# Kernel optimization log

Measured on AMD Instinct MI355X. Metric: run time of the kernel, lower is better.

The kernel has to match this reference:

```python
import jax, jax.numpy as jnp
import numpy as np

N = 32          # agents_num
IN_DIM = 16     # node feature dim (excluding 2 pos cols)
HID = 128
HEADS = 4
OUT = 5
DUEL_H = 256
RADIUS = 0.3
LATENT = HID + HID * HEADS * 2  # 1152
BS = 128


def _lin(k, i, o):
    s = 1.0 / np.sqrt(i)
    return jax.random.uniform(k, (i, o), minval=-s, maxval=s, dtype=jnp.float32)


def setup_inputs() -> dict:
    key = jax.random.key(0)
    ks = jax.random.split(key, 16)
    pos = jax.random.uniform(ks[0], (BS, N, 2))
    feats = jax.random.normal(ks[1], (BS, N, IN_DIM))
    aidx = jax.random.randint(ks[2], (BS,), 0, N).astype(jnp.float32)
    node = jnp.concatenate([pos, feats], axis=-1).reshape(BS, N * (2 + IN_DIM))
    obs = jnp.concatenate([node, aidx[:, None]], axis=1)  # (BS, N*(2+IN_DIM)+1)
    return {
        "obs": obs,
        "enc_w1": _lin(ks[3], IN_DIM, HID), "enc_b1": jnp.zeros((HID,)),
        "enc_w2": _lin(ks[4], HID, HID), "enc_b2": jnp.zeros((HID,)),
        "wl1": _lin(ks[5], HID, HEADS * HID), "wr1": _lin(ks[6], HID, HEADS * HID),
        "att1": jax.random.normal(ks[7], (HEADS, HID)) * 0.1, "bias1": jnp.zeros((HEADS * HID,)),
        "wl2": _lin(ks[8], HID * HEADS, HEADS * HID), "wr2": _lin(ks[9], HID * HEADS, HEADS * HID),
        "att2": jax.random.normal(ks[10], (HEADS, HID)) * 0.1, "bias2": jnp.zeros((HEADS * HID,)),
        "q_w1": _lin(ks[11], LATENT, DUEL_H), "q_b1": jnp.zeros((DUEL_H,)),
        "q_w2": _lin(ks[12], DUEL_H, OUT), "q_b2": jnp.zeros((OUT,)),
        "v_w1": _lin(ks[13], LATENT, DUEL_H), "v_b1": jnp.zeros((DUEL_H,)),
        "v_w2": _lin(ks[14], DUEL_H, 1), "v_b2": jnp.zeros((1,)),
    }


def _gatv2(x, adj, wl, wr, att, bias):
    # Dense-masked GATv2 (PyG semantics: lin_l on source j, lin_r on target i,
    # leaky_relu(x_i + x_j) . att, softmax over neighbors j, aggregate lin_l(x_j)).
    bs, n, _ = x.shape
    gl = (x @ wl).reshape(bs, n, HEADS, HID)  # source transform
    gr = (x @ wr).reshape(bs, n, HEADS, HID)  # target transform
    e = jax.nn.leaky_relu(gr[:, :, None] + gl[:, None, :], 0.2)  # [b, i, j, h, c]
    logits = jnp.einsum('bijhc,hc->bijh', e, att)
    logits = jnp.where(adj[..., None], logits, -jnp.inf)  # diag always True (self loops)
    alpha = jax.nn.softmax(logits, axis=2)
    out = jnp.einsum('bijh,bjhc->bihc', alpha, gl).reshape(bs, n, HEADS * HID)
    return out + bias


def reference(obs, enc_w1, enc_b1, enc_w2, enc_b2,
              wl1, wr1, att1, bias1, wl2, wr2, att2, bias2,
              q_w1, q_b1, q_w2, q_b2, v_w1, v_b1, v_w2, v_b2):
    bs = obs.shape[0]
    node = obs[:, :-1].reshape(bs, N, 2 + IN_DIM)
    pos, feats = node[..., :2], node[..., 2:]
    aidx = jnp.clip(obs[:, -1], 0, N - 1).astype(jnp.int32)

    # radius_graph (per-graph, loop=False) + GATv2 add_self_loops => diag True
    d2 = jnp.sum((pos[:, :, None] - pos[:, None, :]) ** 2, axis=-1)  # [bs, N, N]
    adj = (d2 < RADIUS ** 2) | jnp.eye(N, dtype=bool)

    # encoder MLP then ReLU (as in forward)
    h = jax.nn.relu(feats @ enc_w1 + enc_b1)
    x = jax.nn.relu(h @ enc_w2 + enc_b2)  # [bs, N, HID]

    b = jnp.arange(bs)
    x1 = x[b, aidx]  # [bs, HID]

    x = jax.nn.relu(_gatv2(x, adj, wl1, wr1, att1, bias1))  # [bs, N, HID*HEADS]
    x2 = x[b, aidx]

    x = jax.nn.relu(_gatv2(x, adj, wl2, wr2, att2, bias2))
    x3 = x[b, aidx]

    x_cat = jnp.concatenate([x1, x2, x3], axis=1)  # [bs, LATENT]

    q = jax.nn.relu(x_cat @ q_w1 + q_b1) @ q_w2 + q_b2  # [bs, OUT]
    v = jax.nn.relu(x_cat @ v_w1 + v_b1) @ v_w2 + v_b2  # [bs, 1]
    return q - q.mean(axis=1, keepdims=True) + v
```

## Files before the change

### kernel.cpp

```cpp
#include <hip/hip_runtime.h>
#include <hip/hip_bf16.h>

typedef unsigned int uint_t;
typedef unsigned short ushort_t;
typedef __attribute__((ext_vector_type(8))) short short8;
typedef __attribute__((ext_vector_type(4))) float floatx4;

__device__ __forceinline__ float4 fma4(float4 a, float s, float4 w){
  a.x += s*w.x; a.y += s*w.y; a.z += s*w.z; a.w += s*w.w; return a;
}
__device__ __forceinline__ float4 relu4(float4 a){
  return make_float4(fmaxf(a.x,0.f),fmaxf(a.y,0.f),fmaxf(a.z,0.f),fmaxf(a.w,0.f));
}
__device__ __forceinline__ unsigned bf16rne(float f){
  unsigned u = __float_as_uint(f);
  return (u + 0x7fffu + ((u>>16)&1u)) >> 16;
}
__device__ __forceinline__ uint_t packbf(float f){
  unsigned hb = bf16rne(f);
  float hf = __uint_as_float(hb<<16);
  unsigned lb = bf16rne(f - hf);
  return (hb<<16) | lb;
}
__device__ __forceinline__ uint4 pack4(float4 v){
  uint4 u; u.x=packbf(v.x); u.y=packbf(v.y); u.z=packbf(v.z); u.w=packbf(v.w); return u;
}
__device__ __forceinline__ float unpk(uint_t u){
  return __uint_as_float(u & 0xffff0000u) + __uint_as_float(u<<16);
}
#define UNPACK8(u0,u1,hi,lo) \
  hi[0]=(short)(u0.x>>16); lo[0]=(short)u0.x; \
  hi[1]=(short)(u0.y>>16); lo[1]=(short)u0.y; \
  hi[2]=(short)(u0.z>>16); lo[2]=(short)u0.z; \
  hi[3]=(short)(u0.w>>16); lo[3]=(short)u0.w; \
  hi[4]=(short)(u1.x>>16); lo[4]=(short)u1.x; \
  hi[5]=(short)(u1.y>>16); lo[5]=(short)u1.y; \
  hi[6]=(short)(u1.z>>16); lo[6]=(short)u1.z; \
  hi[7]=(short)(u1.w>>16); lo[7]=(short)u1.w;


template<int NKC>
__device__ __forceinline__ void hgemm_body(
    const uint_t* __restrict__ xcatpk,
    const ushort_t* __restrict__ qw1Thi, const ushort_t* __restrict__ qw1Tlo,
    const ushort_t* __restrict__ vw1Thi, const ushort_t* __restrict__ vw1Tlo,
    float* __restrict__ part, int ks, int ct, int t, int k0c, int slot0)
{
  const int w = t>>6, lane = t&63, m = lane&15, quad = lane>>4;
  const ushort_t* Bhi = (ct<4) ? qw1Thi : vw1Thi;
  const int cbl = (ct<4) ? ct*64 : (ct-4)*64;
  const int cbg = (ct<4) ? ct*64 : 256 + (ct-4)*64;
  const int kb = k0c + ks*NKC;
  const uint_t* ap = xcatpk + (size_t)w*18432 + m*32 + quad*8 + (size_t)kb*512;
  const ushort_t* bp0 = Bhi + (size_t)((cbl>>4)+0)*18432 + m*32 + quad*8 + (size_t)kb*512;
  const ushort_t* bp1 = Bhi + (size_t)((cbl>>4)+1)*18432 + m*32 + quad*8 + (size_t)kb*512;
  const ushort_t* bp2 = Bhi + (size_t)((cbl>>4)+2)*18432 + m*32 + quad*8 + (size_t)kb*512;
  const ushort_t* bp3 = Bhi + (size_t)((cbl>>4)+3)*18432 + m*32 + quad*8 + (size_t)kb*512;
  const size_t lod = (size_t)(qw1Tlo - qw1Thi);
  floatx4 acc[4];
  #pragma unroll
  for (int i=0;i<4;i++) acc[i] = (floatx4){0.f,0.f,0.f,0.f};
  #pragma unroll
  for (int kc=0; kc<NKC; kc++){
    const uint4 ua0 = *(const uint4*)(ap);
    const uint4 ua1 = *(const uint4*)(ap+4);
    ap += 512;
    short8 ahi, alo;
    UNPACK8(ua0,ua1,ahi,alo)
    const ushort_t* bps[4] = {bp0, bp1, bp2, bp3};
    #pragma unroll
    for (int nt=0; nt<4; nt++){
      const short8 bh = *(const short8*)(bps[nt] + kc*512);
      const short8 bl = *(const short8*)(bps[nt] + kc*512 + lod);
      acc[nt] = __builtin_amdgcn_mfma_f32_16x16x32_bf16(ahi, bh, acc[nt], 0,0,0);
      acc[nt] = __builtin_amdgcn_mfma_f32_16x16x32_bf16(ahi, bl, acc[nt], 0,0,0);
      acc[nt] = __builtin_amdgcn_mfma_f32_16x16x32_bf16(alo, bh, acc[nt], 0,0,0);
    }
  }
  float* pdst = part + (size_t)(slot0+ks)*65536;
  const int crow0 = w*16 + quad*4;
  #pragma unroll
  for (int nt=0; nt<4; nt++){
    const int col = cbg + nt*16 + m;
    #pragma unroll
    for (int r=0;r<4;r++)
      pdst[(size_t)(crow0 + r)*512 + col] = acc[nt][r];
  }
}

__global__ __launch_bounds__(256) void prep_kernel(
    const float* __restrict__ obs,
    const float* __restrict__ enc_w1, const float* __restrict__ enc_b1,
    const float* __restrict__ enc_w2, const float* __restrict__ enc_b2,
    const float* __restrict__ wl1, const float* __restrict__ wr1,
    const float* __restrict__ wl2, const float* __restrict__ wr2,
    const float* __restrict__ q_w1, const float* __restrict__ v_w1,
    ushort_t* __restrict__ wl1Thi, ushort_t* __restrict__ wl1Tlo,
    ushort_t* __restrict__ wr1Thi, ushort_t* __restrict__ wr1Tlo,
    ushort_t* __restrict__ wl2Thi, ushort_t* __restrict__ wl2Tlo,
    ushort_t* __restrict__ wr2Thi, ushort_t* __restrict__ wr2Tlo,
    ushort_t* __restrict__ qw1Thi, ushort_t* __restrict__ qw1Tlo,
    ushort_t* __restrict__ vw1Thi, ushort_t* __restrict__ vw1Tlo,
    uint_t* __restrict__ xpk, uint_t* __restrict__ xcatpk,
    unsigned* __restrict__ adjw, int* __restrict__ aiw)
{
  const int t = threadIdx.x, bid = blockIdx.x;
  if (bid >= 512){
    __shared__ float sm[32][33];
    const int cw = bid - 512;
    const float* in; ushort_t* ohi; ushort_t* olo; int K, N, tt, ktiles;
    if (cw < 64)       { in=wl1;  ohi=wl1Thi; olo=wl1Tlo; K=128;  N=512; tt=cw;     ktiles=4;  }
    else if (cw < 128) { in=wr1;  ohi=wr1Thi; olo=wr1Tlo; K=128;  N=512; tt=cw-64;  ktiles=4;  }
    else if (cw < 384) { in=wl2;  ohi=wl2Thi; olo=wl2Tlo; K=512;  N=512; tt=cw-128; ktiles=16; }
    else if (cw < 640) { in=wr2;  ohi=wr2Thi; olo=wr2Tlo; K=512;  N=512; tt=cw-384; ktiles=16; }
    else if (cw < 800) { in=q_w1; ohi=qw1Thi; olo=qw1Tlo; K=1152; N=256; tt=cw-640; ktiles=20; }
    else               { in=v_w1; ohi=vw1Thi; olo=vw1Tlo; K=1152; N=256; tt=cw-800; ktiles=20; }
    const int kt = tt % ktiles, nt = tt / ktiles;
    const int r = t>>5, c = t&31;
    #pragma unroll
    for (int i=0;i<4;i++)
      sm[r+i*8][c] = in[(size_t)(kt*32 + r + i*8)*N + nt*32 + c];
    __syncthreads();
    #pragma unroll
    for (int i=0;i<4;i++){
      const int nl = r + i*8;
      const int n  = nt*32 + nl;
      const float f = sm[c][nl];
      const unsigned hb = bf16rne(f);
      const float hf = __uint_as_float(hb<<16);
      const unsigned lb = bf16rne(f - hf);
      const size_t off = (size_t)(n>>4)*(size_t)(16*K) + (size_t)kt*512 + (size_t)(n&15)*32 + c;
      ohi[off] = (ushort_t)hb;
      olo[off] = (ushort_t)lb;
    }
    return;
  }
  __shared__ float s_pos[64];
  __shared__ float s_feats[128];
  __shared__ __align__(16) float s_h[8*132];
  __shared__ int s_ai;
  const int s = bid & 127, g = bid >> 7;
  const float* ob = obs + s*577;

  if (t==0){
    float a = ob[576];
    a = fminf(fmaxf(a, 0.f), 31.f);
    s_ai = (int)a;
    if (g==0) aiw[s] = (int)a;
  }
  if (t < 128){ const int n=t>>4, f=t&15; s_feats[t] = ob[(g*8+n)*18+2+f]; }
  if (g==0 && t>=128 && t<192){ const int u=t-128; s_pos[u] = ob[(u>>1)*18 + (u&1)]; }
  __syncthreads();

  if (g==0 && t < 32){
    const float px = s_pos[2*t], py = s_pos[2*t+1];
    const float R2 = 0.09f;
    unsigned mm = 0u;
    for (int j=0;j<32;j++){
      const float dx = __fsub_rn(px, s_pos[2*j]), dy = __fsub_rn(py, s_pos[2*j+1]);
      const float d2 = __fadd_rn(__fmul_rn(dx,dx), __fmul_rn(dy,dy));
      if (d2 <= R2 || j==t) mm |= (1u<<j);
    }
    adjw[s*32+t] = mm;
  }

  const int n = t>>5, c0 = (t&31)*4;
  {
    float4 a = *(const float4*)(enc_b1+c0);
    #pragma unroll
    for (int f=0; f<16; f++)
      a = fma4(a, s_feats[n*16+f], *(const float4*)(enc_w1 + f*128 + c0));
    *(float4*)&s_h[n*132+c0] = relu4(a);
  }
  __syncthreads();
  {
    float4 a = *(const float4*)(enc_b2+c0);
    #pragma unroll 4
    for (int k=0;k<128;k+=4){
      const float4 hv = *(const float4*)&s_h[n*132+k];
      a = fma4(a, hv.x, *(const float4*)(enc_w2 + (k+0)*128 + c0));
      a = fma4(a, hv.y, *(const float4*)(enc_w2 + (k+1)*128 + c0));
      a = fma4(a, hv.z, *(const float4*)(enc_w2 + (k+2)*128 + c0));
      a = fma4(a, hv.w, *(const float4*)(enc_w2 + (k+3)*128 + c0));
    }
    a = relu4(a);
    const uint4 p = pack4(a);
    const int i = g*8 + n;
    uint_t* xp = xpk + (size_t)(s*2 + (i>>4))*2048 + (c0>>5)*512 + (i&15)*32 + (c0&31);
    *(uint4*)xp = p;
    if (i == s_ai){
      uint_t* xc = xcatpk + (size_t)(s>>4)*18432 + (c0>>5)*512 + (s&15)*32 + (c0&31);
      *(uint4*)xc = p;
    }
  }
}

__global__ __launch_bounds__(512) void pa1_kernel(
    const uint_t* __restrict__ xpk,
    const ushort_t* __restrict__ wl1Thi, const ushort_t* __restrict__ wl1Tlo,
    const ushort_t* __restrict__ wr1Thi, const ushort_t* __restrict__ wr1Tlo,
    const float* __restrict__ att, const float* __restrict__ bias,
    const unsigned* __restrict__ adjw, const int* __restrict__ aiw,
    uint_t* __restrict__ x2pk, uint_t* __restrict__ xcatpk)
{
  __shared__ __align__(16) uint_t s_ax[4096];
  __shared__ __align__(16) float s_gl[32*132];
  __shared__ __align__(16) float s_gr[32*132];
  __shared__ __align__(16) float s_att[128];
  __shared__ __align__(16) float s_b[128];
  __shared__ float s_lg[32*33];
  __shared__ unsigned s_adj[32];
  const int t = threadIdx.x, bid = blockIdx.x;

  const int s = bid & 127, h = bid >> 7;
  const int w = t>>6, lane = t&63, m = lane&15, quad = lane>>4;
  const int mat = w>>2, cpair = w&3;

  if (t < 128){ s_att[t] = att[h*128 + t]; s_b[t] = bias[h*128 + t]; }
  if (t >= 224 && t < 256) s_adj[t-224] = adjw[s*32 + (t-224)];
  const int ai = aiw[s];

  #pragma unroll
  for (int j=0;j<2;j++){
    const int W = t*8 + j*4;
    const int kcl = W>>10, rp = (W>>9)&1, u = W&511;
    const int du = u ^ (((u>>5)&7)<<2);
    *(uint4*)&s_ax[kcl*1024 + rp*512 + du] =
      *(const uint4*)(xpk + (size_t)(s*2+rp)*2048 + (size_t)kcl*512 + u);
  }

  const ushort_t* Bhi = (mat==0) ? wl1Thi : wr1Thi;
  const ushort_t* Blo = (mat==0) ? wl1Tlo : wr1Tlo;
  const int nbase = h*8 + cpair*2;
  const ushort_t* bp0 = Bhi + (size_t)(nbase+0)*2048 + m*32 + quad*8;
  const ushort_t* bp1 = Bhi + (size_t)(nbase+1)*2048 + m*32 + quad*8;
  const size_t lod = (size_t)(Blo - Bhi);
  const int sw = (m*32 + quad*8) ^ ((m&7)<<2);
  floatx4 acc[2][2];
  #pragma unroll
  for (int i=0;i<2;i++)
    #pragma unroll
    for (int j=0;j<2;j++) acc[i][j] = (floatx4){0.f,0.f,0.f,0.f};

  __syncthreads();

  #pragma unroll
  for (int kc=0; kc<4; kc++){
    const uint4 u00 = *(const uint4*)&s_ax[kc*1024 + sw];
    const uint4 u01 = *(const uint4*)&s_ax[kc*1024 + (sw^4)];
    const uint4 u10 = *(const uint4*)&s_ax[kc*1024 + 512 + sw];
    const uint4 u11 = *(const uint4*)&s_ax[kc*1024 + 512 + (sw^4)];
    short8 ahi0, alo0, ahi1, alo1;
    UNPACK8(u00,u01,ahi0,alo0)
    UNPACK8(u10,u11,ahi1,alo1)
    const ushort_t* bps[2] = {bp0, bp1};
    #pragma unroll
    for (int nt=0; nt<2; nt++){
      const short8 bh = *(const short8*)(bps[nt] + kc*512);
      const short8 bl = *(const short8*)(bps[nt] + kc*512 + lod);
      acc[0][nt] = __builtin_amdgcn_mfma_f32_16x16x32_bf16(ahi0, bh, acc[0][nt], 0,0,0);
      acc[0][nt] = __builtin_amdgcn_mfma_f32_16x16x32_bf16(ahi0, bl, acc[0][nt], 0,0,0);
      acc[0][nt] = __builtin_amdgcn_mfma_f32_16x16x32_bf16(alo0, bh, acc[0][nt], 0,0,0);
      acc[1][nt] = __builtin_amdgcn_mfma_f32_16x16x32_bf16(ahi1, bh, acc[1][nt], 0,0,0);
      acc[1][nt] = __builtin_amdgcn_mfma_f32_16x16x32_bf16(ahi1, bl, acc[1][nt], 0,0,0);
      acc[1][nt] = __builtin_amdgcn_mfma_f32_16x16x32_bf16(alo1, bh, acc[1][nt], 0,0,0);
    }
  }
  {
    float* dst = mat ? s_gr : s_gl;
    const int colbase = cpair*32;
    #pragma unroll
    for (int nt=0; nt<2; nt++){
      const int col = colbase + nt*16 + m;
      #pragma unroll
      for (int r=0;r<4;r++){
        dst[(quad*4+r)*132 + col]      = acc[0][nt][r];
        dst[(16+quad*4+r)*132 + col]   = acc[1][nt][r];
      }
    }
  }
  __syncthreads();

  {
    const int i = t>>4, jb = t&15;
    float lacc[2] = {0.f,0.f};
    for (int c=0;c<128;c+=4){
      const float4 g = *(const float4*)&s_gr[i*132+c];
      const float4 a = *(const float4*)&s_att[c];
      #pragma unroll
      for (int mm=0;mm<2;mm++){
        const float4 gj = *(const float4*)&s_gl[(jb+16*mm)*132 + c];
        float ex = g.x+gj.x; ex = fmaxf(ex, 0.2f*ex);
        float ey = g.y+gj.y; ey = fmaxf(ey, 0.2f*ey);
        float ez = g.z+gj.z; ez = fmaxf(ez, 0.2f*ez);
        float ew = g.w+gj.w; ew = fmaxf(ew, 0.2f*ew);
        lacc[mm] += ex*a.x + ey*a.y + ez*a.z + ew*a.w;
      }
    }
    s_lg[i*33 + jb]      = lacc[0];
    s_lg[i*33 + jb + 16] = lacc[1];
  }
  __syncthreads();

  #pragma unroll
  for (int rnd=0; rnd<2; rnd++){
    const int i = rnd*16 + (t>>5), j = t&31;
    const float lg = s_lg[i*33+j];
    const bool ok = (s_adj[i]>>j)&1u;
    float v = ok ? lg : -3.0e38f;
    #pragma unroll
    for (int d_=16; d_; d_>>=1) v = fmaxf(v, __shfl_xor(v, d_, 32));
    const float e = ok ? __expf(lg - v) : 0.f;
    float sum = e;
    #pragma unroll
    for (int d_=16; d_; d_>>=1) sum += __shfl_xor(sum, d_, 32);
    s_lg[i*33+j] = e / sum;
  }
  __syncthreads();

  {
    const int i = t>>4, c0 = (t&15)*8;
    float4 o0 = make_float4(0.f,0.f,0.f,0.f), o1 = o0;
    for (int j=0;j<32;j++){
      const float al = s_lg[i*33+j];
      o0 = fma4(o0, al, *(const float4*)&s_gl[j*132 + c0]);
      o1 = fma4(o1, al, *(const float4*)&s_gl[j*132 + c0 + 4]);
    }
    const float4 b0 = *(const float4*)&s_b[c0];
    const float4 b1 = *(const float4*)&s_b[c0+4];
    o0 = relu4(make_float4(o0.x+b0.x, o0.y+b0.y, o0.z+b0.z, o0.w+b0.w));
    o1 = relu4(make_float4(o1.x+b1.x, o1.y+b1.y, o1.z+b1.z, o1.w+b1.w));
    const uint4 p0 = pack4(o0), p1 = pack4(o1);
    const int kb = h*128 + c0;
    uint_t* xp = x2pk + (size_t)(s*2 + (i>>4))*8192 + (kb>>5)*512 + (i&15)*32 + (kb&31);
    *(uint4*)&xp[0] = p0;
    *(uint4*)&xp[4] = p1;
    if (i == ai){
      const int kk = 128 + kb;
      uint_t* tp = xcatpk + (size_t)(s>>4)*18432 + (kk>>5)*512 + (s&15)*32 + (kk&31);
      *(uint4*)&tp[0] = p0;
      *(uint4*)&tp[4] = p1;
    }
  }
}

__global__ __launch_bounds__(512) void pa2_kernel(
    const uint_t* __restrict__ x2pk, const uint_t* __restrict__ xcatpk,
    const ushort_t* __restrict__ wl2Thi, const ushort_t* __restrict__ wl2Tlo,
    const ushort_t* __restrict__ wr2Thi, const ushort_t* __restrict__ wr2Tlo,
    const ushort_t* __restrict__ qw1Thi, const ushort_t* __restrict__ qw1Tlo,
    const ushort_t* __restrict__ vw1Thi, const ushort_t* __restrict__ vw1Tlo,
    const float* __restrict__ att2, const float* __restrict__ bias2,
    const unsigned* __restrict__ adjw, const int* __restrict__ aiw,
    const float* __restrict__ q_w1, const float* __restrict__ v_w1,
    float* __restrict__ hpart, float* __restrict__ hp3)
{
  __shared__ __align__(16) uint_t s_a[8192];
  __shared__ __align__(16) float s_gl[32*132];
  __shared__ __align__(16) float s_p2[128];
  __shared__ __align__(16) float s_at[128];
  __shared__ __align__(16) float s_bb[128];
  __shared__ float s_lg[32];
  __shared__ float s_al[32];
  const int t = threadIdx.x, bid = blockIdx.x;

  if (bid >= 512){
    const int hk = bid - 512;
    hgemm_body<5>(xcatpk, qw1Thi, qw1Tlo, vw1Thi, vw1Tlo, hpart, hk>>3, hk&7, t, 0, 0);
    return;
  }

  const int s = bid & 127, h = bid >> 7;
  const int w = t>>6, lane = t&63, m = lane&15, quad = lane>>4;
  (void)lane;
  const int ai = aiw[s];
  const unsigned arow = adjw[s*32+ai];
  const int sw = (m*32 + quad*8) ^ ((m&7)<<2);

  if (t < 128){ s_at[t] = att2[h*128+t]; s_bb[t] = bias2[h*128+t]; }

  {
    const int rt = s >> 4;
    #pragma unroll
    for (int j=0;j<4;j++){
      const int W = t*16 + j*4;
      const int kcl = W>>9, u = W&511;
      const int du = u ^ (((u>>5)&7)<<2);
      *(uint4*)&s_a[kcl*512 + du] =
        *(const uint4*)(xcatpk + (size_t)rt*18432 + (size_t)(4+kcl)*512 + u);
    }
  }
  __syncthreads();
  {
    const int ct = h*8 + w;
    const ushort_t* bp = wr2Thi + (size_t)ct*8192 + m*32 + quad*8;
    const size_t lodr = (size_t)(wr2Tlo - wr2Thi);
    floatx4 acc = (floatx4){0.f,0.f,0.f,0.f};
    #pragma unroll 4
    for (int kc=0; kc<16; kc++){
      const uint4 ua0 = *(const uint4*)&s_a[kc*512 + sw];
      const uint4 ua1 = *(const uint4*)&s_a[kc*512 + (sw^4)];
      short8 ahi, alo;
      UNPACK8(ua0,ua1,ahi,alo)
      const short8 bh = *(const short8*)(bp + kc*512);
      const short8 bl = *(const short8*)(bp + kc*512 + lodr);
      acc = __builtin_amdgcn_mfma_f32_16x16x32_bf16(ahi, bh, acc, 0,0,0);
      acc = __builtin_amdgcn_mfma_f32_16x16x32_bf16(ahi, bl, acc, 0,0,0);
      acc = __builtin_amdgcn_mfma_f32_16x16x32_bf16(alo, bh, acc, 0,0,0);
    }
    #pragma unroll
    for (int r=0;r<4;r++)
      s_gl[(quad*4+r)*132 + w*16 + m] = acc[r];
  }
  __syncthreads();
  if (t < 128) s_p2[t] = s_gl[(s&15)*132 + t];
  __syncthreads();

  const ushort_t* bq = wl2Thi + (size_t)(h*8 + w)*8192 + m*32 + quad*8;
  const size_t lod = (size_t)(wl2Tlo - wl2Thi);
  floatx4 acc0 = (floatx4){0.f,0.f,0.f,0.f}, acc1 = acc0;

  #pragma unroll
  for (int half=0; half<2; half++){
    #pragma unroll
    for (int j=0;j<4;j++){
      const int W = t*16 + j*4;
      const int kcl = W>>10, rp = (W>>9)&1, u = W&511;
      const int du = u ^ (((u>>5)&7)<<2);
      *(uint4*)&s_a[kcl*1024 + rp*512 + du] =
        *(const uint4*)(x2pk + (size_t)(s*2+rp)*8192 + (size_t)(half*8+kcl)*512 + u);
    }
    __syncthreads();
    #pragma unroll 4
    for (int kcl=0; kcl<8; kcl++){
      const int kc = half*8 + kcl;
      const uint4 u00 = *(const uint4*)&s_a[kcl*1024 + sw];
      const uint4 u01 = *(const uint4*)&s_a[kcl*1024 + (sw^4)];
      const uint4 u10 = *(const uint4*)&s_a[kcl*1024 + 512 + sw];
      const uint4 u11 = *(const uint4*)&s_a[kcl*1024 + 512 + (sw^4)];
      short8 ahi0, alo0, ahi1, alo1;
      UNPACK8(u00,u01,ahi0,alo0)
      UNPACK8(u10,u11,ahi1,alo1)
      const short8 bh = *(const short8*)(bq + kc*512);
      const short8 bl = *(const short8*)(bq + kc*512 + lod);
      acc0 = __builtin_amdgcn_mfma_f32_16x16x32_bf16(ahi0, bh, acc0, 0,0,0);
      acc0 = __builtin_amdgcn_mfma_f32_16x16x32_bf16(ahi0, bl, acc0, 0,0,0);
      acc0 = __builtin_amdgcn_mfma_f32_16x16x32_bf16(alo0, bh, acc0, 0,0,0);
      acc1 = __builtin_amdgcn_mfma_f32_16x16x32_bf16(ahi1, bh, acc1, 0,0,0);
      acc1 = __builtin_amdgcn_mfma_f32_16x16x32_bf16(ahi1, bl, acc1, 0,0,0);
      acc1 = __builtin_amdgcn_mfma_f32_16x16x32_bf16(alo1, bh, acc1, 0,0,0);
    }
    __syncthreads();
  }
  {
    const int col = w*16 + m;
    #pragma unroll
    for (int r=0;r<4;r++){
      s_gl[(quad*4+r)*132 + col]    = acc0[r];
      s_gl[(16+quad*4+r)*132 + col] = acc1[r];
    }
  }
  __syncthreads();

  if (t < 256){
    const int j = t>>3, pq = t&7;
    float sum = 0.f;
    #pragma unroll
    for (int q=0;q<4;q++){
      const int c = pq*16 + q*4;
      const float4 g = *(const float4*)&s_gl[j*132 + c];
      const float4 r = *(const float4*)&s_p2[c];
      const float4 a = *(const float4*)&s_at[c];
      float e0 = r.x+g.x; e0 = fmaxf(e0, 0.2f*e0);
      float e1 = r.y+g.y; e1 = fmaxf(e1, 0.2f*e1);
      float e2 = r.z+g.z; e2 = fmaxf(e2, 0.2f*e2);
      float e3 = r.w+g.w; e3 = fmaxf(e3, 0.2f*e3);
      sum += e0*a.x + e1*a.y + e2*a.z + e3*a.w;
    }
    sum += __shfl_xor(sum,1,64);
    sum += __shfl_xor(sum,2,64);
    sum += __shfl_xor(sum,4,64);
    if (pq==0) s_lg[j] = sum;
  }
  __syncthreads();
  if (t < 32){
    const float lg = s_lg[t];
    const bool ok = (arow>>t)&1u;
    float v = ok ? lg : -3.0e38f;
    #pragma unroll
    for (int d_=16; d_; d_>>=1) v = fmaxf(v, __shfl_xor(v, d_, 32));
    const float e = ok ? __expf(lg - v) : 0.f;
    float sm = e;
    #pragma unroll
    for (int d_=16; d_; d_>>=1) sm += __shfl_xor(sm, d_, 32);
    s_al[t] = e / sm;
  }
  __syncthreads();
  if (t < 128){
    float acc2 = 0.f;
    #pragma unroll 8
    for (int j=0;j<32;j++) acc2 += s_al[j] * s_gl[j*132 + t];
    s_p2[t] = fmaxf(acc2 + s_bb[t], 0.f);
  }
  __syncthreads();

  {
    const float* Wm = (t < 256) ? q_w1 : v_w1;
    const int col = t & 255;
    const float* wp = Wm + (size_t)(640 + h*128)*256 + col;
    float acc3 = 0.f;
    #pragma unroll 8
    for (int k=0;k<128;k++) acc3 += s_p2[k] * wp[(size_t)k*256];
    hp3[((size_t)h*128 + s)*512 + t] = acc3;
  }
}

__global__ __launch_bounds__(256) void hepi_kernel(
    const float* __restrict__ hpart, const float* __restrict__ hp3,
    const float* __restrict__ q_b1, const float* __restrict__ q_w2, const float* __restrict__ q_b2,
    const float* __restrict__ v_b1, const float* __restrict__ v_w2, const float* __restrict__ v_b2,
    float* __restrict__ out)
{
  __shared__ float s_p[4*6];
  const int t = threadIdx.x, s = blockIdx.x;
  float hq = q_b1[t], hv = v_b1[t];
  #pragma unroll
  for (int ks=0; ks<4; ks++){
    hq += hpart[(size_t)ks*65536 + (size_t)s*512 + t];
    hv += hpart[(size_t)ks*65536 + (size_t)s*512 + 256 + t];
  }
  #pragma unroll
  for (int h=0; h<4; h++){
    hq += hp3[((size_t)h*128 + s)*512 + t];
    hv += hp3[((size_t)h*128 + s)*512 + 256 + t];
  }
  hq = fmaxf(hq, 0.f);
  hv = fmaxf(hv, 0.f);
  float p[6];
  #pragma unroll
  for (int o=0;o<5;o++) p[o] = hq * q_w2[t*5+o];
  p[5] = hv * v_w2[t];
  #pragma unroll
  for (int d_=32; d_; d_>>=1){
    #pragma unroll
    for (int o=0;o<6;o++) p[o] += __shfl_xor(p[o], d_, 64);
  }
  const int w = t>>6, lane = t&63;
  if (lane==0){
    #pragma unroll
    for (int o=0;o<6;o++) s_p[w*6+o] = p[o];
  }
  __syncthreads();
  if (t < 6) s_p[t] = s_p[t] + s_p[6+t] + s_p[12+t] + s_p[18+t];
  __syncthreads();
  if (t < 5){
    const float q0 = s_p[0]+q_b2[0], q1 = s_p[1]+q_b2[1], q2 = s_p[2]+q_b2[2],
                q3 = s_p[3]+q_b2[3], q4 = s_p[4]+q_b2[4];
    const float mean = (q0+q1+q2+q3+q4) / 5.0f;
    const float v = s_p[5] + v_b2[0];
    const float qt = (t==0?q0:t==1?q1:t==2?q2:t==3?q3:q4);
    out[s*5+t] = qt - mean + v;
  }
}

extern "C" void kernel_launch(void* const* d_in, const int* in_sizes, int n_in,
                              void* d_out, int out_size, void* d_ws, size_t ws_size,
                              hipStream_t stream) {
  (void)n_in; (void)out_size; (void)ws_size;
  const float* obs    = (const float*)d_in[0];
  const float* enc_w1 = (const float*)d_in[1];
  const float* enc_b1 = (const float*)d_in[2];
  const float* enc_w2 = (const float*)d_in[3];
  const float* enc_b2 = (const float*)d_in[4];
  const float* wl1    = (const float*)d_in[5];
  const float* wr1    = (const float*)d_in[6];
  const float* att1   = (const float*)d_in[7];
  const float* bias1  = (const float*)d_in[8];
  const float* wl2    = (const float*)d_in[9];
  const float* wr2    = (const float*)d_in[10];
  const float* att2   = (const float*)d_in[11];
  const float* bias2  = (const float*)d_in[12];
  const float* q_w1   = (const float*)d_in[13];
  const float* q_b1   = (const float*)d_in[14];
  const float* q_w2   = (const float*)d_in[15];
  const float* q_b2   = (const float*)d_in[16];
  const float* v_w1   = (const float*)d_in[17];
  const float* v_b1   = (const float*)d_in[18];
  const float* v_w2   = (const float*)d_in[19];
  const float* v_b2   = (const float*)d_in[20];

  char* ws = (char*)d_ws;
  uint_t*   x_pk    = (uint_t*)  (ws + 0);
  uint_t*   xcat_pk = (uint_t*)  (ws + 2097152);
  unsigned* adjw    = (unsigned*)(ws + 2686976);
  int*      aiw     = (int*)     (ws + 2703360);
  uint_t*   x2_pk   = (uint_t*)  (ws + 2703872);
  ushort_t* wl1Thi  = (ushort_t*)(ws + 11092480);
  ushort_t* wl1Tlo  = (ushort_t*)(ws + 11223552);
  ushort_t* wr1Thi  = (ushort_t*)(ws + 11354624);
  ushort_t* wr1Tlo  = (ushort_t*)(ws + 11485696);
  ushort_t* wl2Thi  = (ushort_t*)(ws + 11616768);
  ushort_t* wl2Tlo  = (ushort_t*)(ws + 12141056);
  ushort_t* qw1Thi  = (ushort_t*)(ws + 12665344);
  ushort_t* qw1Tlo  = (ushort_t*)(ws + 13255168);
  ushort_t* vw1Thi  = (ushort_t*)(ws + 13844992);
  ushort_t* vw1Tlo  = (ushort_t*)(ws + 14434816);
  ushort_t* wr2Thi  = (ushort_t*)(ws + 15024640);
  ushort_t* wr2Tlo  = (ushort_t*)(ws + 15548928);
  float*    hpart   = (float*)   (ws + 16073216);
  float*    hp3     = (float*)   (ws + 17121792);

  prep_kernel<<<512 + 960, 256, 0, stream>>>(obs, enc_w1, enc_b1, enc_w2, enc_b2,
      wl1, wr1, wl2, wr2, q_w1, v_w1,
      wl1Thi, wl1Tlo, wr1Thi, wr1Tlo, wl2Thi, wl2Tlo, wr2Thi, wr2Tlo,
      qw1Thi, qw1Tlo, vw1Thi, vw1Tlo,
      x_pk, xcat_pk, adjw, aiw);

  pa1_kernel<<<512, 512, 0, stream>>>(x_pk, wl1Thi, wl1Tlo, wr1Thi, wr1Tlo,
      att1, bias1, adjw, aiw, x2_pk, xcat_pk);

  pa2_kernel<<<512 + 32, 512, 0, stream>>>(x2_pk, xcat_pk,
      wl2Thi, wl2Tlo, wr2Thi, wr2Tlo,
      qw1Thi, qw1Tlo, vw1Thi, vw1Tlo,
      att2, bias2, adjw, aiw, q_w1, v_w1,
      hpart, hp3);

  hepi_kernel<<<128, 256, 0, stream>>>(hpart, hp3,
      q_b1, q_w2, q_b2, v_b1, v_w2, v_b2,
      (float*)d_out);
}
```

Baseline: 161.8 us.

## Move layer-2 and head weight conversion from prep kernel into pa1 kernel

The bf16 hi/lo split-and-transpose of wl2, wr2, q_w1 and v_w1 moves out of prep_kernel into extra blocks (832 of them, 512 threads each) appended to pa1_kernel. Those weights are only needed by pa2, so the conversion can run alongside the layer-1 attention instead of lengthening the critical-path prep kernel. It reuses pa1's s_gl shared buffer as the transpose scratch. The cost is that the extra conversion blocks now compete with the attention blocks for compute units.

```diff
diff --git a/kernel.cpp b/kernel.cpp
--- a/kernel.cpp
+++ b/kernel.cpp
@@ -93,14 +93,8 @@
     const float* __restrict__ enc_w1, const float* __restrict__ enc_b1,
     const float* __restrict__ enc_w2, const float* __restrict__ enc_b2,
     const float* __restrict__ wl1, const float* __restrict__ wr1,
-    const float* __restrict__ wl2, const float* __restrict__ wr2,
-    const float* __restrict__ q_w1, const float* __restrict__ v_w1,
     ushort_t* __restrict__ wl1Thi, ushort_t* __restrict__ wl1Tlo,
     ushort_t* __restrict__ wr1Thi, ushort_t* __restrict__ wr1Tlo,
-    ushort_t* __restrict__ wl2Thi, ushort_t* __restrict__ wl2Tlo,
-    ushort_t* __restrict__ wr2Thi, ushort_t* __restrict__ wr2Tlo,
-    ushort_t* __restrict__ qw1Thi, ushort_t* __restrict__ qw1Tlo,
-    ushort_t* __restrict__ vw1Thi, ushort_t* __restrict__ vw1Tlo,
     uint_t* __restrict__ xpk, uint_t* __restrict__ xcatpk,
     unsigned* __restrict__ adjw, int* __restrict__ aiw)
 {
@@ -108,13 +102,11 @@
   if (bid >= 512){
     __shared__ float sm[32][33];
     const int cw = bid - 512;
-    const float* in; ushort_t* ohi; ushort_t* olo; int K, N, tt, ktiles;
-    if (cw < 64)       { in=wl1;  ohi=wl1Thi; olo=wl1Tlo; K=128;  N=512; tt=cw;     ktiles=4;  }
-    else if (cw < 128) { in=wr1;  ohi=wr1Thi; olo=wr1Tlo; K=128;  N=512; tt=cw-64;  ktiles=4;  }
-    else if (cw < 384) { in=wl2;  ohi=wl2Thi; olo=wl2Tlo; K=512;  N=512; tt=cw-128; ktiles=16; }
-    else if (cw < 640) { in=wr2;  ohi=wr2Thi; olo=wr2Tlo; K=512;  N=512; tt=cw-384; ktiles=16; }
-    else if (cw < 800) { in=q_w1; ohi=qw1Thi; olo=qw1Tlo; K=1152; N=256; tt=cw-640; ktiles=20; }
-    else               { in=v_w1; ohi=vw1Thi; olo=vw1Tlo; K=1152; N=256; tt=cw-800; ktiles=20; }
+    const float* in; ushort_t* ohi; ushort_t* olo; int tt;
+    const int K = 128, N = 512;
+    if (cw < 64){ in=wl1; ohi=wl1Thi; olo=wl1Tlo; tt=cw; }
+    else        { in=wr1; ohi=wr1Thi; olo=wr1Tlo; tt=cw-64; }
+    const int ktiles = K>>5;
     const int kt = tt % ktiles, nt = tt / ktiles;
     const int r = t>>5, c = t&31;
     #pragma unroll
@@ -201,6 +193,12 @@
     const ushort_t* __restrict__ wr1Thi, const ushort_t* __restrict__ wr1Tlo,
     const float* __restrict__ att, const float* __restrict__ bias,
     const unsigned* __restrict__ adjw, const int* __restrict__ aiw,
+    const float* __restrict__ wl2, const float* __restrict__ wr2,
+    const float* __restrict__ q_w1, const float* __restrict__ v_w1,
+    ushort_t* __restrict__ wl2Thi, ushort_t* __restrict__ wl2Tlo,
+    ushort_t* __restrict__ wr2Thi, ushort_t* __restrict__ wr2Tlo,
+    ushort_t* __restrict__ qw1Thi, ushort_t* __restrict__ qw1Tlo,
+    ushort_t* __restrict__ vw1Thi, ushort_t* __restrict__ vw1Tlo,
     uint_t* __restrict__ x2pk, uint_t* __restrict__ xcatpk)
 {
   __shared__ __align__(16) uint_t s_ax[4096];
@@ -211,6 +209,34 @@
   __shared__ float s_lg[32*33];
   __shared__ unsigned s_adj[32];
   const int t = threadIdx.x, bid = blockIdx.x;
+
+  if (bid >= 512){
+    const int cw = bid - 512;
+    const float* in; ushort_t* ohi; ushort_t* olo; int K, N, tt, ktiles;
+    if (cw < 256)      { in=wl2;  ohi=wl2Thi; olo=wl2Tlo; K=512;  N=512; tt=cw;     ktiles=16; }
+    else if (cw < 512) { in=wr2;  ohi=wr2Thi; olo=wr2Tlo; K=512;  N=512; tt=cw-256; ktiles=16; }
+    else if (cw < 672) { in=q_w1; ohi=qw1Thi; olo=qw1Tlo; K=1152; N=256; tt=cw-512; ktiles=20; }
+    else               { in=v_w1; ohi=vw1Thi; olo=vw1Tlo; K=1152; N=256; tt=cw-672; ktiles=20; }
+    const int kt = tt % ktiles, nt = tt / ktiles;
+    const int r = t>>5, c = t&31;
+    #pragma unroll
+    for (int i=0;i<2;i++)
+      s_gl[(r+i*16)*33 + c] = in[(size_t)(kt*32 + r + i*16)*N + nt*32 + c];
+    __syncthreads();
+    #pragma unroll
+    for (int i=0;i<2;i++){
+      const int nl = r + i*16;
+      const int n  = nt*32 + nl;
+      const float f = s_gl[c*33 + nl];
+      const unsigned hb = bf16rne(f);
+      const float hf = __uint_as_float(hb<<16);
+      const unsigned lb = bf16rne(f - hf);
+      const size_t off = (size_t)(n>>4)*(size_t)(16*K) + (size_t)kt*512 + (size_t)(n&15)*32 + c;
+      ohi[off] = (ushort_t)hb;
+      olo[off] = (ushort_t)lb;
+    }
+    return;
+  }
 
   const int s = bid & 127, h = bid >> 7;
   const int w = t>>6, lane = t&63, m = lane&15, quad = lane>>4;
@@ -610,14 +636,16 @@
   float*    hpart   = (float*)   (ws + 16073216);
   float*    hp3     = (float*)   (ws + 17121792);
 
-  prep_kernel<<<512 + 960, 256, 0, stream>>>(obs, enc_w1, enc_b1, enc_w2, enc_b2,
-      wl1, wr1, wl2, wr2, q_w1, v_w1,
-      wl1Thi, wl1Tlo, wr1Thi, wr1Tlo, wl2Thi, wl2Tlo, wr2Thi, wr2Tlo,
-      qw1Thi, qw1Tlo, vw1Thi, vw1Tlo,
+  prep_kernel<<<512 + 128, 256, 0, stream>>>(obs, enc_w1, enc_b1, enc_w2, enc_b2,
+      wl1, wr1,
+      wl1Thi, wl1Tlo, wr1Thi, wr1Tlo,
       x_pk, xcat_pk, adjw, aiw);
 
-  pa1_kernel<<<512, 512, 0, stream>>>(x_pk, wl1Thi, wl1Tlo, wr1Thi, wr1Tlo,
-      att1, bias1, adjw, aiw, x2_pk, xcat_pk);
+  pa1_kernel<<<512 + 832, 512, 0, stream>>>(x_pk, wl1Thi, wl1Tlo, wr1Thi, wr1Tlo,
+      att1, bias1, adjw, aiw,
+      wl2, wr2, q_w1, v_w1,
+      wl2Thi, wl2Tlo, wr2Thi, wr2Tlo, qw1Thi, qw1Tlo, vw1Thi, vw1Tlo,
+      x2_pk, xcat_pk);
 
   pa2_kernel<<<512 + 32, 512, 0, stream>>>(x2_pk, xcat_pk,
       wl2Thi, wl2Tlo, wr2Thi, wr2Tlo,
```

Result: no change. 164.1 us (+1.4%).

## Fuse encoder MLP and adjacency build into the first GAT kernel

Applied to the files above, without the earlier changes.

Moves the encoder MLP, the radius adjacency mask and the agent-index extraction out of the prep kernel and into pa1_kernel, which now writes the packed encoder output straight into shared memory. This drops the global round trip through x_pk and leaves the prep kernel doing only the weight conversion. In exchange the encoder is recomputed four times, once per head block, since each of the 512 blocks redoes it for its sample.

```diff
diff --git a/kernel.cpp b/kernel.cpp
--- a/kernel.cpp
+++ b/kernel.cpp
@@ -88,10 +88,7 @@
   }
 }
 
-__global__ __launch_bounds__(256) void prep_kernel(
-    const float* __restrict__ obs,
-    const float* __restrict__ enc_w1, const float* __restrict__ enc_b1,
-    const float* __restrict__ enc_w2, const float* __restrict__ enc_b2,
+__global__ __launch_bounds__(256) void conv_kernel(
     const float* __restrict__ wl1, const float* __restrict__ wr1,
     const float* __restrict__ wl2, const float* __restrict__ wr2,
     const float* __restrict__ q_w1, const float* __restrict__ v_w1,
@@ -100,107 +97,45 @@
     ushort_t* __restrict__ wl2Thi, ushort_t* __restrict__ wl2Tlo,
     ushort_t* __restrict__ wr2Thi, ushort_t* __restrict__ wr2Tlo,
     ushort_t* __restrict__ qw1Thi, ushort_t* __restrict__ qw1Tlo,
-    ushort_t* __restrict__ vw1Thi, ushort_t* __restrict__ vw1Tlo,
-    uint_t* __restrict__ xpk, uint_t* __restrict__ xcatpk,
-    unsigned* __restrict__ adjw, int* __restrict__ aiw)
+    ushort_t* __restrict__ vw1Thi, ushort_t* __restrict__ vw1Tlo)
 {
-  const int t = threadIdx.x, bid = blockIdx.x;
-  if (bid >= 512){
-    __shared__ float sm[32][33];
-    const int cw = bid - 512;
-    const float* in; ushort_t* ohi; ushort_t* olo; int K, N, tt, ktiles;
-    if (cw < 64)       { in=wl1;  ohi=wl1Thi; olo=wl1Tlo; K=128;  N=512; tt=cw;     ktiles=4;  }
-    else if (cw < 128) { in=wr1;  ohi=wr1Thi; olo=wr1Tlo; K=128;  N=512; tt=cw-64;  ktiles=4;  }
-    else if (cw < 384) { in=wl2;  ohi=wl2Thi; olo=wl2Tlo; K=512;  N=512; tt=cw-128; ktiles=16; }
-    else if (cw < 640) { in=wr2;  ohi=wr2Thi; olo=wr2Tlo; K=512;  N=512; tt=cw-384; ktiles=16; }
-    else if (cw < 800) { in=q_w1; ohi=qw1Thi; olo=qw1Tlo; K=1152; N=256; tt=cw-640; ktiles=20; }
-    else               { in=v_w1; ohi=vw1Thi; olo=vw1Tlo; K=1152; N=256; tt=cw-800; ktiles=20; }
-    const int kt = tt % ktiles, nt = tt / ktiles;
-    const int r = t>>5, c = t&31;
-    #pragma unroll
-    for (int i=0;i<4;i++)
-      sm[r+i*8][c] = in[(size_t)(kt*32 + r + i*8)*N + nt*32 + c];
-    __syncthreads();
-    #pragma unroll
-    for (int i=0;i<4;i++){
-      const int nl = r + i*8;
-      const int n  = nt*32 + nl;
-      const float f = sm[c][nl];
-      const unsigned hb = bf16rne(f);
-      const float hf = __uint_as_float(hb<<16);
-      const unsigned lb = bf16rne(f - hf);
-      const size_t off = (size_t)(n>>4)*(size_t)(16*K) + (size_t)kt*512 + (size_t)(n&15)*32 + c;
-      ohi[off] = (ushort_t)hb;
-      olo[off] = (ushort_t)lb;
-    }
-    return;
-  }
-  __shared__ float s_pos[64];
-  __shared__ float s_feats[128];
-  __shared__ __align__(16) float s_h[8*132];
-  __shared__ int s_ai;
-  const int s = bid & 127, g = bid >> 7;
-  const float* ob = obs + s*577;
-
-  if (t==0){
-    float a = ob[576];
-    a = fminf(fmaxf(a, 0.f), 31.f);
-    s_ai = (int)a;
-    if (g==0) aiw[s] = (int)a;
-  }
-  if (t < 128){ const int n=t>>4, f=t&15; s_feats[t] = ob[(g*8+n)*18+2+f]; }
-  if (g==0 && t>=128 && t<192){ const int u=t-128; s_pos[u] = ob[(u>>1)*18 + (u&1)]; }
-  __syncthreads();
-
-  if (g==0 && t < 32){
-    const float px = s_pos[2*t], py = s_pos[2*t+1];
-    const float R2 = 0.09f;
-    unsigned mm = 0u;
-    for (int j=0;j<32;j++){
-      const float dx = __fsub_rn(px, s_pos[2*j]), dy = __fsub_rn(py, s_pos[2*j+1]);
-      const float d2 = __fadd_rn(__fmul_rn(dx,dx), __fmul_rn(dy,dy));
-      if (d2 <= R2 || j==t) mm |= (1u<<j);
-    }
-    adjw[s*32+t] = mm;
-  }
-
-  const int n = t>>5, c0 = (t&31)*4;
-  {
-    float4 a = *(const float4*)(enc_b1+c0);
-    #pragma unroll
-    for (int f=0; f<16; f++)
-      a = fma4(a, s_feats[n*16+f], *(const float4*)(enc_w1 + f*128 + c0));
-    *(float4*)&s_h[n*132+c0] = relu4(a);
-  }
-  __syncthreads();
-  {
-    float4 a = *(const float4*)(enc_b2+c0);
-    #pragma unroll 4
-    for (int k=0;k<128;k+=4){
-      const float4 hv = *(const float4*)&s_h[n*132+k];
-      a = fma4(a, hv.x, *(const float4*)(enc_w2 + (k+0)*128 + c0));
-      a = fma4(a, hv.y, *(const float4*)(enc_w2 + (k+1)*128 + c0));
-      a = fma4(a, hv.z, *(const float4*)(enc_w2 + (k+2)*128 + c0));
-      a = fma4(a, hv.w, *(const float4*)(enc_w2 + (k+3)*128 + c0));
-    }
-    a = relu4(a);
-    const uint4 p = pack4(a);
-    const int i = g*8 + n;
-    uint_t* xp = xpk + (size_t)(s*2 + (i>>4))*2048 + (c0>>5)*512 + (i&15)*32 + (c0&31);
-    *(uint4*)xp = p;
-    if (i == s_ai){
-      uint_t* xc = xcatpk + (size_t)(s>>4)*18432 + (c0>>5)*512 + (s&15)*32 + (c0&31);
-      *(uint4*)xc = p;
-    }
+  __shared__ float sm[32][33];
+  const int t = threadIdx.x, cw = blockIdx.x;
+  const float* in; ushort_t* ohi; ushort_t* olo; int K, N, tt, ktiles;
+  if (cw < 64)       { in=wl1;  ohi=wl1Thi; olo=wl1Tlo; K=128;  N=512; tt=cw;     ktiles=4;  }
+  else if (cw < 128) { in=wr1;  ohi=wr1Thi; olo=wr1Tlo; K=128;  N=512; tt=cw-64;  ktiles=4;  }
+  else if (cw < 384) { in=wl2;  ohi=wl2Thi; olo=wl2Tlo; K=512;  N=512; tt=cw-128; ktiles=16; }
+  else if (cw < 640) { in=wr2;  ohi=wr2Thi; olo=wr2Tlo; K=512;  N=512; tt=cw-384; ktiles=16; }
+  else if (cw < 800) { in=q_w1; ohi=qw1Thi; olo=qw1Tlo; K=1152; N=256; tt=cw-640; ktiles=20; }
+  else               { in=v_w1; ohi=vw1Thi; olo=vw1Tlo; K=1152; N=256; tt=cw-800; ktiles=20; }
+  const int kt = tt % ktiles, nt = tt / ktiles;
+  const int r = t>>5, c = t&31;
+  #pragma unroll
+  for (int i=0;i<4;i++)
+    sm[r+i*8][c] = in[(size_t)(kt*32 + r + i*8)*N + nt*32 + c];
+  __syncthreads();
+  #pragma unroll
+  for (int i=0;i<4;i++){
+    const int nl = r + i*8;
+    const int n  = nt*32 + nl;
+    const float f = sm[c][nl];
+    const unsigned hb = bf16rne(f);
+    const float hf = __uint_as_float(hb<<16);
+    const unsigned lb = bf16rne(f - hf);
+    const size_t off = (size_t)(n>>4)*(size_t)(16*K) + (size_t)kt*512 + (size_t)(n&15)*32 + c;
+    ohi[off] = (ushort_t)hb;
+    olo[off] = (ushort_t)lb;
   }
 }
 
 __global__ __launch_bounds__(512) void pa1_kernel(
-    const uint_t* __restrict__ xpk,
+    const float* __restrict__ obs,
+    const float* __restrict__ enc_w1, const float* __restrict__ enc_b1,
+    const float* __restrict__ enc_w2, const float* __restrict__ enc_b2,
     const ushort_t* __restrict__ wl1Thi, const ushort_t* __restrict__ wl1Tlo,
     const ushort_t* __restrict__ wr1Thi, const ushort_t* __restrict__ wr1Tlo,
     const float* __restrict__ att, const float* __restrict__ bias,
-    const unsigned* __restrict__ adjw, const int* __restrict__ aiw,
+    unsigned* __restrict__ adjw, int* __restrict__ aiw,
     uint_t* __restrict__ x2pk, uint_t* __restrict__ xcatpk)
 {
   __shared__ __align__(16) uint_t s_ax[4096];
@@ -210,23 +145,81 @@
   __shared__ __align__(16) float s_b[128];
   __shared__ float s_lg[32*33];
   __shared__ unsigned s_adj[32];
+  __shared__ float s_pos[64];
+  __shared__ float s_feats[512];
+  __shared__ int s_ai;
   const int t = threadIdx.x, bid = blockIdx.x;
 
   const int s = bid & 127, h = bid >> 7;
   const int w = t>>6, lane = t&63, m = lane&15, quad = lane>>4;
   const int mat = w>>2, cpair = w&3;
-
+  const float* ob = obs + s*577;
+
+  if (t==0){
+    float a = ob[576];
+    a = fminf(fmaxf(a, 0.f), 31.f);
+    s_ai = (int)a;
+    if (h==0) aiw[s] = (int)a;
+  }
+  s_feats[t] = ob[(t>>4)*18 + 2 + (t&15)];
+  if (t < 64) s_pos[t] = ob[(t>>1)*18 + (t&1)];
   if (t < 128){ s_att[t] = att[h*128 + t]; s_b[t] = bias[h*128 + t]; }
-  if (t >= 224 && t < 256) s_adj[t-224] = adjw[s*32 + (t-224)];
-  const int ai = aiw[s];
-
-  #pragma unroll
-  for (int j=0;j<2;j++){
-    const int W = t*8 + j*4;
-    const int kcl = W>>10, rp = (W>>9)&1, u = W&511;
-    const int du = u ^ (((u>>5)&7)<<2);
-    *(uint4*)&s_ax[kcl*1024 + rp*512 + du] =
-      *(const uint4*)(xpk + (size_t)(s*2+rp)*2048 + (size_t)kcl*512 + u);
+  __syncthreads();
+
+  if (t < 32){
+    const float px = s_pos[2*t], py = s_pos[2*t+1];
+    const float R2 = 0.09f;
+    unsigned mm = 0u;
+    for (int j=0;j<32;j++){
+      const float dx = __fsub_rn(px, s_pos[2*j]), dy = __fsub_rn(py, s_pos[2*j+1]);
+      const float d2 = __fadd_rn(__fmul_rn(dx,dx), __fmul_rn(dy,dy));
+      if (d2 <= R2 || j==t) mm |= (1u<<j);
+    }
+    s_adj[t] = mm;
+    if (h==0) adjw[s*32+t] = mm;
+  }
+
+  const int n = t>>4, c0 = (t&15)*8;
+  {
+    float4 a0 = *(const float4*)(enc_b1+c0);
+    float4 a1 = *(const float4*)(enc_b1+c0+4);
+    #pragma unroll
+    for (int f=0; f<16; f++){
+      const float sf = s_feats[n*16+f];
+      a0 = fma4(a0, sf, *(const float4*)(enc_w1 + f*128 + c0));
+      a1 = fma4(a1, sf, *(const float4*)(enc_w1 + f*128 + c0 + 4));
+    }
+    *(float4*)&s_gl[n*132+c0]   = relu4(a0);
+    *(float4*)&s_gl[n*132+c0+4] = relu4(a1);
+  }
+  __syncthreads();
+
+  {
+    float4 a0 = *(const float4*)(enc_b2+c0);
+    float4 a1 = *(const float4*)(enc_b2+c0+4);
+    #pragma unroll 4
+    for (int k=0;k<128;k++){
+      const float hv = s_gl[n*132+k];
+      a0 = fma4(a0, hv, *(const float4*)(enc_w2 + k*128 + c0));
+      a1 = fma4(a1, hv, *(const float4*)(enc_w2 + k*128 + c0 + 4));
+    }
+    a0 = relu4(a0); a1 = relu4(a1);
+    uint_t pk[8];
+    pk[0]=packbf(a0.x); pk[1]=packbf(a0.y); pk[2]=packbf(a0.z); pk[3]=packbf(a0.w);
+    pk[4]=packbf(a1.x); pk[5]=packbf(a1.y); pk[6]=packbf(a1.z); pk[7]=packbf(a1.w);
+    const int kc = c0>>5, rp = n>>4;
+    const int ub = (n&15)*32 + (c0&31);
+    const int xr = (n&7)<<2;
+    #pragma unroll
+    for (int j=0;j<8;j++)
+      s_ax[kc*1024 + rp*512 + ((ub+j)^xr)] = pk[j];
+    if (h==0 && n == s_ai){
+      #pragma unroll
+      for (int j=0;j<8;j++){
+        const int kk = c0 + j;
+        xcatpk[(size_t)(s>>4)*18432 + (size_t)(kk>>5)*512 + (s&15)*32 + (kk&31)] = pk[j];
+      }
+    }
   }
 
   const ushort_t* Bhi = (mat==0) ? wl1Thi : wr1Thi;
@@ -319,23 +312,23 @@
   __syncthreads();
 
   {
-    const int i = t>>4, c0 = (t&15)*8;
+    const int i = t>>4, cc0 = (t&15)*8;
     float4 o0 = make_float4(0.f,0.f,0.f,0.f), o1 = o0;
     for (int j=0;j<32;j++){
       const float al = s_lg[i*33+j];
-      o0 = fma4(o0, al, *(const float4*)&s_gl[j*132 + c0]);
-      o1 = fma4(o1, al, *(const float4*)&s_gl[j*132 + c0 + 4]);
-    }
-    const float4 b0 = *(const float4*)&s_b[c0];
-    const float4 b1 = *(const float4*)&s_b[c0+4];
+      o0 = fma4(o0, al, *(const float4*)&s_gl[j*132 + cc0]);
+      o1 = fma4(o1, al, *(const float4*)&s_gl[j*132 + cc0 + 4]);
+    }
+    const float4 b0 = *(const float4*)&s_b[cc0];
+    const float4 b1 = *(const float4*)&s_b[cc0+4];
     o0 = relu4(make_float4(o0.x+b0.x, o0.y+b0.y, o0.z+b0.z, o0.w+b0.w));
     o1 = relu4(make_float4(o1.x+b1.x, o1.y+b1.y, o1.z+b1.z, o1.w+b1.w));
     const uint4 p0 = pack4(o0), p1 = pack4(o1);
-    const int kb = h*128 + c0;
+    const int kb = h*128 + cc0;
     uint_t* xp = x2pk + (size_t)(s*2 + (i>>4))*8192 + (kb>>5)*512 + (i&15)*32 + (kb&31);
     *(uint4*)&xp[0] = p0;
     *(uint4*)&xp[4] = p1;
-    if (i == ai){
+    if (i == s_ai){
       const int kk = 128 + kb;
       uint_t* tp = xcatpk + (size_t)(s>>4)*18432 + (kk>>5)*512 + (s&15)*32 + (kk&31);
       *(uint4*)&tp[0] = p0;
@@ -590,7 +583,6 @@
   const float* v_b2   = (const float*)d_in[20];
 
   char* ws = (char*)d_ws;
-  uint_t*   x_pk    = (uint_t*)  (ws + 0);
   uint_t*   xcat_pk = (uint_t*)  (ws + 2097152);
   unsigned* adjw    = (unsigned*)(ws + 2686976);
   int*      aiw     = (int*)     (ws + 2703360);
@@ -610,13 +602,12 @@
   float*    hpart   = (float*)   (ws + 16073216);
   float*    hp3     = (float*)   (ws + 17121792);
 
-  prep_kernel<<<512 + 960, 256, 0, stream>>>(obs, enc_w1, enc_b1, enc_w2, enc_b2,
-      wl1, wr1, wl2, wr2, q_w1, v_w1,
+  conv_kernel<<<960, 256, 0, stream>>>(wl1, wr1, wl2, wr2, q_w1, v_w1,
       wl1Thi, wl1Tlo, wr1Thi, wr1Tlo, wl2Thi, wl2Tlo, wr2Thi, wr2Tlo,
-      qw1Thi, qw1Tlo, vw1Thi, vw1Tlo,
-      x_pk, xcat_pk, adjw, aiw);
-
-  pa1_kernel<<<512, 512, 0, stream>>>(x_pk, wl1Thi, wl1Tlo, wr1Thi, wr1Tlo,
+      qw1Thi, qw1Tlo, vw1Thi, vw1Tlo);
+
+  pa1_kernel<<<512, 512, 0, stream>>>(obs, enc_w1, enc_b1, enc_w2, enc_b2,
+      wl1Thi, wl1Tlo, wr1Thi, wr1Tlo,
       att1, bias1, adjw, aiw, x2_pk, xcat_pk);
 
   pa2_kernel<<<512 + 32, 512, 0, stream>>>(x2_pk, xcat_pk,
```

After: 184.3 us. 1.14x slower.
